# Kernel optimization log

Measured on AMD Instinct MI355X. Metric: run time of the kernel, lower is better.

## Reference

```python
import jax, jax.numpy as jnp
import numpy as np

N = 100000   # nodes
E = 1250000  # edges
G = 64       # graphs in batch
F_IN, H, NT, GT = 29, 64, 6, 4
L = 4        # num GCN layers


def setup_inputs() -> dict:
    key = jax.random.key(0)
    ks = jax.random.split(key, 14)
    s_in = 1.0 / np.sqrt(F_IN)
    s_h = 1.0 / np.sqrt(H)
    return {
        "x": jax.random.normal(ks[0], (N, F_IN), dtype=jnp.float32),
        "edge_index": jax.random.randint(ks[1], (2, E), 0, N, dtype=jnp.int64),
        "batch": jnp.sort(jax.random.randint(ks[2], (N,), 0, G, dtype=jnp.int64)),
        "encW": jax.random.uniform(ks[3], (F_IN, H), jnp.float32, -s_in, s_in),
        "encb": jax.random.uniform(ks[4], (H,), jnp.float32, -s_in, s_in),
        "convW": jax.random.uniform(ks[5], (L, H, H), jnp.float32, -s_h, s_h),
        "convb": jax.random.uniform(ks[6], (L, H), jnp.float32, -s_h, s_h),
        "nodeW": jax.random.uniform(ks[7], (H, NT), jnp.float32, -s_h, s_h),
        "nodeb": jax.random.uniform(ks[8], (NT,), jnp.float32, -s_h, s_h),
        "g1W": jax.random.uniform(ks[9], (H, H), jnp.float32, -s_h, s_h),
        "g1b": jax.random.uniform(ks[10], (H,), jnp.float32, -s_h, s_h),
        "g2W": jax.random.uniform(ks[11], (H, GT), jnp.float32, -s_h, s_h),
        "g2b": jax.random.uniform(ks[12], (GT,), jnp.float32, -s_h, s_h),
    }


def reference(x, edge_index, batch, encW, encb, convW, convb, nodeW, nodeb, g1W, g1b, g2W, g2b):
    # GCNConv with self-loops and symmetric normalization (PyG defaults)
    loop = jnp.arange(N, dtype=edge_index.dtype)
    row = jnp.concatenate([edge_index[0], loop])  # senders
    col = jnp.concatenate([edge_index[1], loop])  # receivers
    deg = jax.ops.segment_sum(jnp.ones_like(col, dtype=x.dtype), col, num_segments=N)
    dis = jnp.where(deg > 0, deg ** -0.5, 0.0)
    norm = (dis[row] * dis[col])[:, None]  # [E+N, 1]

    h = jax.nn.relu(x @ encW + encb)
    for i in range(L):
        hw = h @ convW[i]  # transform then propagate
        agg = jax.ops.segment_sum(hw[row] * norm, col, num_segments=N)
        h = jax.nn.relu(agg + convb[i])

    pred_node = h @ nodeW + nodeb

    counts = jax.ops.segment_sum(jnp.ones((N,), x.dtype), batch, num_segments=G)
    gemb = jax.ops.segment_sum(h, batch, num_segments=G) / jnp.maximum(counts, 1.0)[:, None]
    pred_global = jax.nn.relu(gemb @ g1W + g1b) @ g2W + g2b
    return (pred_node, pred_global)
```

## Files before the change

kernel.cpp:

```cpp
#include <hip/hip_runtime.h>
#include <hip/hip_fp16.h>

#define N_NODES 100000
#define N_EDGES 1250000
#define N_GRAPHS 64
#define F_INN 29
#define HD 64
#define NT 6
#define GT 4
#define NLAYERS 4
#define RECS_CAP 3000000
#define NBLK 1563
#define NBUK 782
#define HGRID 256
#define GB_BLOCKS 391
#define ENC_BLOCKS 6250
#define NH_BLOCKS 3125

typedef __attribute__((ext_vector_type(8))) _Float16 f16x8;
typedef __attribute__((ext_vector_type(4))) float f32x4;

__global__ void hist1_misc(const int* __restrict__ col, int* __restrict__ ghistT, int E,
                           const float* __restrict__ convW, uint4* __restrict__ wfrag,
                           __half* __restrict__ ht1, __half* __restrict__ ht2,
                           const int* __restrict__ batch, int* __restrict__ start) {
    __shared__ int lh[NBUK];
    int tid = threadIdx.x, b = blockIdx.x;
    if (b < HGRID) {
        for (int i = tid; i < NBUK; i += 256) lh[i] = 0;
        __syncthreads();
        for (int e = b * 256 + tid; e < E; e += HGRID * 256) atomicAdd(&lh[col[e] >> 7], 1);
        __syncthreads();
        for (int i = tid; i < NBUK; i += 256) ghistT[i * 256 + b] = lh[i];
    } else if (b < HGRID + 4) {
        int layer = b - HGRID;
        const float* W = convW + (size_t)layer * HD * HD;
        uint4* out = wfrag + (size_t)layer * 512;
        for (int s = tid; s < 512; s += 256) {
            int jt = s >> 7, ks = (s >> 6) & 1, l = s & 63;
            int j = jt * 16 + (l & 15);
            int k0 = ks * 32 + (l >> 4) * 8;
            __align__(16) __half hh[8];
            #pragma unroll
            for (int i = 0; i < 8; ++i) hh[i] = __float2half_rn(W[(size_t)(k0 + i) * HD + j]);
            out[s] = *reinterpret_cast<const uint4*>(hh);
        }
    } else if (b == HGRID + 4) {
        if (tid < HD) ht1[(size_t)N_NODES * HD + tid] = __float2half_rn(0.f);
        else if (tid < 2 * HD) ht2[(size_t)N_NODES * HD + (tid - HD)] = __float2half_rn(0.f);
    } else {
        int i = (b - HGRID - 5) * 256 + tid;
        if (i < N_NODES) {
            int bb = batch[i];
            if (i == 0) {
                for (int g = 0; g <= bb; ++g) start[g] = 0;
            } else {
                int pb = batch[i - 1];
                if (pb != bb) for (int g = pb + 1; g <= bb; ++g) start[g] = i;
            }
            if (i == N_NODES - 1) {
                for (int g = bb + 1; g <= N_GRAPHS; ++g) start[g] = N_NODES;
            }
        }
    }
}

__global__ void hist_colscan(int* __restrict__ ghistT, int* __restrict__ tot) {
    __shared__ int wsum[4];
    int k = blockIdx.x, tid = threadIdx.x;
    int v = ghistT[k * 256 + tid];
    int incl = v;
    int lane = tid & 63;
    #pragma unroll
    for (int off = 1; off < 64; off <<= 1) {
        int t = __shfl_up(incl, (unsigned)off, 64);
        if (lane >= off) incl += t;
    }
    if (lane == 63) wsum[tid >> 6] = incl;
    __syncthreads();
    int woff = 0;
    for (int w = 0; w < (tid >> 6); ++w) woff += wsum[w];
    ghistT[k * 256 + tid] = woff + incl - v;
    if (tid == 255) tot[k] = woff + incl;
}

__global__ void scan1(const int* __restrict__ in, int* __restrict__ out,
                      int* __restrict__ bsums, int n) {
    __shared__ int wsum[4];
    int tid = threadIdx.x;
    int base = blockIdx.x * 1024 + tid * 4;
    int v0 = (base + 0 < n) ? in[base + 0] : 0;
    int v1 = (base + 1 < n) ? in[base + 1] : 0;
    int v2 = (base + 2 < n) ? in[base + 2] : 0;
    int v3 = (base + 3 < n) ? in[base + 3] : 0;
    int tsum = v0 + v1 + v2 + v3;
    int incl = tsum;
    int lane = tid & 63;
    #pragma unroll
    for (int off = 1; off < 64; off <<= 1) {
        int t = __shfl_up(incl, (unsigned)off, 64);
        if (lane >= off) incl += t;
    }
    if (lane == 63) wsum[tid >> 6] = incl;
    __syncthreads();
    int woff = 0;
    for (int w = 0; w < (tid >> 6); ++w) woff += wsum[w];
    int run = woff + incl - tsum;
    if (base + 0 < n) out[base + 0] = run; run += v0;
    if (base + 1 < n) out[base + 1] = run; run += v1;
    if (base + 2 < n) out[base + 2] = run; run += v2;
    if (base + 3 < n) out[base + 3] = run;
    if (tid == 255) bsums[blockIdx.x] = woff + incl;
}

__global__ void scatter_buckets(const int* __restrict__ row, const int* __restrict__ col,
                                const int* __restrict__ ghistT, const int* __restrict__ boff,
                                unsigned* __restrict__ bke, int E) {
    __shared__ int cur[NBUK];
    int tid = threadIdx.x, b = blockIdx.x;
    for (int i = tid; i < NBUK; i += 256) cur[i] = ghistT[i * 256 + b] + boff[i];
    __syncthreads();
    for (int e = b * 256 + tid; e < E; e += HGRID * 256) {
        int c = col[e];
        int pos = atomicAdd(&cur[c >> 7], 1);
        bke[pos] = (unsigned)row[e] | ((unsigned)(c & 127) << 25);
    }
}

__global__ void bucket_count(const unsigned* __restrict__ bke, const int* __restrict__ boff,
                             int* __restrict__ cnt16, float* __restrict__ dis,
                             int* __restrict__ btot, int E) {
    __shared__ int lc[128];
    __shared__ int red[2];
    int k = blockIdx.x, tid = threadIdx.x;
    if (tid < 128) lc[tid] = 0;
    __syncthreads();
    int s = boff[k];
    int t = (k == NBUK - 1) ? E : boff[k + 1];
    for (int i = s + tid; i < t; i += 256) atomicAdd(&lc[bke[i] >> 25], 1);
    __syncthreads();
    int c16 = 0;
    if (tid < 128) {
        int node = k * 128 + tid;
        if (node < N_NODES) {
            int c = lc[tid];
            c16 = (c + 15) & ~15;
            cnt16[node] = c16;
            dis[node] = rsqrtf((float)(c + 1));
        }
        int sum = c16;
        #pragma unroll
        for (int off = 1; off < 64; off <<= 1) sum += __shfl_xor(sum, off, 64);
        if ((tid & 63) == 0) red[tid >> 6] = sum;
    }
    __syncthreads();
    if (tid == 0) btot[k] = red[0] + red[1];
}

__global__ void fill_enc(const unsigned* __restrict__ bke, const int* __restrict__ boff,
                         const int* __restrict__ bbase, const int* __restrict__ cnt16,
                         int* __restrict__ offs, int* __restrict__ srcs, int E,
                         const float* __restrict__ x, const float* __restrict__ encW,
                         const float* __restrict__ encb, const float* __restrict__ dis,
                         __half* __restrict__ ht) {
    int tid = threadIdx.x;
    int b = blockIdx.x;
    if (b < NBUK) {
        __shared__ int offsL[128];
        __shared__ int cur[128];
        __shared__ int wtot[2];
        int k = b;
        int v = 0, incl = 0;
        if (tid < 128) {
            int node = k * 128 + tid;
            v = (node < N_NODES) ? cnt16[node] : 0;
            incl = v;
            int lane = tid & 63;
            #pragma unroll
            for (int off = 1; off < 64; off <<= 1) {
                int t = __shfl_up(incl, (unsigned)off, 64);
                if (lane >= off) incl += t;
            }
            if (lane == 63) wtot[tid >> 6] = incl;
        }
        __syncthreads();
        if (tid < 128) {
            int w0 = (tid >= 64) ? wtot[0] : 0;
            int node = k * 128 + tid;
            int o = bbase[k] + w0 + incl - v;
            offsL[tid] = o;
            cur[tid] = 0;
            if (node < N_NODES) offs[node] = o;
        }
        __syncthreads();
        int s = boff[k];
        int t = (k == NBUK - 1) ? E : boff[k + 1];
        for (int i = s + tid; i < t; i += 256) {
            unsigned u = bke[i];
            int l = u >> 25;
            int r = atomicAdd(&cur[l], 1);
            srcs[offsL[l] + r] = (int)(u & 0x01FFFFFFu);
        }
        __syncthreads();
        if (tid < 128) {
            int node = k * 128 + tid;
            if (node < N_NODES) {
                int c = cur[tid];
                int c16 = (c + 15) & ~15;
                int base = offsL[tid];
                for (int p = base + c; p < base + c16; ++p) srcs[p] = N_NODES;
            }
        }
    } else {
        __shared__ float Ws[F_INN * HD];
        __shared__ float bs[HD];
        __shared__ float xs[16 * F_INN];
        for (int i = tid; i < F_INN * HD; i += 256) Ws[i] = encW[i];
        if (tid < HD) bs[tid] = encb[tid];
        int n0 = (b - NBUK) * 16;
        for (int i = tid; i < 16 * F_INN; i += 256) {
            int nn = n0 + i / F_INN;
            xs[i] = (nn < N_NODES) ? x[(size_t)nn * F_INN + (i % F_INN)] : 0.f;
        }
        __syncthreads();
        #pragma unroll
        for (int it = 0; it < 4; ++it) {
            int l = it * 4 + (tid >> 6);
            int j = tid & 63;
            int nn = n0 + l;
            if (nn < N_NODES) {
                float a = bs[j];
                #pragma unroll
                for (int k = 0; k < F_INN; ++k) a = fmaf(xs[l * F_INN + k], Ws[k * HD + j], a);
                ht[(size_t)nn * HD + j] = __float2half_rn(dis[nn] * fmaxf(a, 0.f));
            }
        }
    }
}


__device__ __forceinline__ float4 cvtrow(uint2 u) {
    float2 a = __half22float2(*reinterpret_cast<const __half2*>(&u.x));
    float2 b = __half22float2(*reinterpret_cast<const __half2*>(&u.y));
    return make_float4(a.x, a.y, b.x, b.y);
}

#define ROW16(src) (*reinterpret_cast<const uint2*>(&ht[(size_t)(src) * HD + fh]))
#define H2(u) (*reinterpret_cast<const __half2*>(&(u)))
#define ACC4T(r0, r1, r2, r3) { \
    __half2 ax = __hadd2(__hadd2(H2(r0.x), H2(r1.x)), __hadd2(H2(r2.x), H2(r3.x))); \
    __half2 ay = __hadd2(__hadd2(H2(r0.y), H2(r1.y)), __hadd2(H2(r2.y), H2(r3.y))); \
    float2 fx = __half22float2(ax); \
    float2 fy = __half22float2(ay); \
    acc.x += fx.x; acc.y += fx.y; acc.z += fy.x; acc.w += fy.y; }

__global__ void layer_kernel(const __half* __restrict__ ht,
                             const int* __restrict__ offs, const int* __restrict__ cnt16,
                             const int4* __restrict__ srcs4,
                             const float* __restrict__ dis,
                             const uint4* __restrict__ wfragL, const float* __restrict__ bias,
                             __half* __restrict__ hout, int scaleOut) {
    __shared__ uint4 WfS[512];
    __shared__ __half aggS[64 * 72];
    __shared__ int offsS[64];
    __shared__ int cntS[64];
    __shared__ float disS[64];
    __shared__ float biasS[64];
    int tid = threadIdx.x;
    int b = blockIdx.x;
    WfS[tid] = wfragL[tid];
    WfS[tid + 256] = wfragL[tid + 256];
    if (tid < 64) {
        int d = b * 64 + tid;
        biasS[tid] = bias[tid];
        if (d < N_NODES) {
            offsS[tid] = offs[d];
            cntS[tid] = cnt16[d];
            disS[tid] = dis[d];
        } else {
            offsS[tid] = offs[N_NODES - 1] + cnt16[N_NODES - 1];
            cntS[tid] = 0;
            disS[tid] = 0.f;
        }
    }
    __syncthreads();

    int wave = tid >> 6;
    int lane = tid & 63;
    int q = lane >> 4;
    int fh = (lane & 15) * 4;

    int l0 = wave * 16 + q * 4;
    {
        int nbase = b * 64 + l0;
        *reinterpret_cast<uint2*>(&aggS[(l0 + 0) * 72 + fh]) = ROW16(min(nbase + 0, N_NODES));
        *reinterpret_cast<uint2*>(&aggS[(l0 + 1) * 72 + fh]) = ROW16(min(nbase + 1, N_NODES));
        *reinterpret_cast<uint2*>(&aggS[(l0 + 2) * 72 + fh]) = ROW16(min(nbase + 2, N_NODES));
        *reinterpret_cast<uint2*>(&aggS[(l0 + 3) * 72 + fh]) = ROW16(min(nbase + 3, N_NODES));
    }
    int s = offsS[l0];
    int e = offsS[l0 + 3] + cntS[l0 + 3];
    int dcur = l0;
    int nb = offsS[l0] + cntS[l0];
    float4 acc = {0.f, 0.f, 0.f, 0.f};

    auto flush = [&](int d) {
        uint2 sv = *reinterpret_cast<uint2*>(&aggS[d * 72 + fh]);
        float4 sf = cvtrow(sv);
        acc.x += sf.x; acc.y += sf.y; acc.z += sf.z; acc.w += sf.w;
        __half2 h0 = __floats2half2_rn(acc.x, acc.y);
        __half2 h1 = __floats2half2_rn(acc.z, acc.w);
        uint2 w;
        w.x = *(unsigned*)&h0;
        w.y = *(unsigned*)&h1;
        *reinterpret_cast<uint2*>(&aggS[d * 72 + fh]) = w;
        acc = make_float4(0.f, 0.f, 0.f, 0.f);
    };

    int4 i0, i1, i2, i3;
    if (s < e) {
        int base = s >> 2;
        i0 = srcs4[base + 0];
        i1 = srcs4[base + 1];
        i2 = srcs4[base + 2];
        i3 = srcs4[base + 3];
    }
    for (int p = s; p < e; p += 16) {
        uint2 r0 = ROW16(i0.x), r1 = ROW16(i0.y), r2 = ROW16(i0.z), r3 = ROW16(i0.w);
        uint2 r4 = ROW16(i1.x), r5 = ROW16(i1.y), r6 = ROW16(i1.z), r7 = ROW16(i1.w);
        uint2 r8 = ROW16(i2.x), r9 = ROW16(i2.y), r10 = ROW16(i2.z), r11 = ROW16(i2.w);
        uint2 r12 = ROW16(i3.x), r13 = ROW16(i3.y), r14 = ROW16(i3.z), r15 = ROW16(i3.w);
        int pn = p + 16;
        if (pn < e) {
            int base = pn >> 2;
            i0 = srcs4[base + 0];
            i1 = srcs4[base + 1];
            i2 = srcs4[base + 2];
            i3 = srcs4[base + 3];
        }
        while (p >= nb) {
            flush(dcur);
            ++dcur;
            nb = offsS[dcur] + cntS[dcur];
        }
        ACC4T(r0, r1, r2, r3);
        ACC4T(r4, r5, r6, r7);
        ACC4T(r8, r9, r10, r11);
        ACC4T(r12, r13, r14, r15);
    }
    while (dcur <= l0 + 3) {
        flush(dcur);
        ++dcur;
    }

    f32x4 c0 = {0.f, 0.f, 0.f, 0.f}, c1 = c0, c2 = c0, c3 = c0;
    #pragma unroll
    for (int ks = 0; ks < 2; ++ks) {
        f16x8 a = *reinterpret_cast<const f16x8*>(
            &aggS[(wave * 16 + (lane & 15)) * 72 + ks * 32 + (lane >> 4) * 8]);
        f16x8 b0 = *reinterpret_cast<const f16x8*>(&WfS[(0 * 2 + ks) * 64 + lane]);
        c0 = __builtin_amdgcn_mfma_f32_16x16x32_f16(a, b0, c0, 0, 0, 0);
        f16x8 b1 = *reinterpret_cast<const f16x8*>(&WfS[(1 * 2 + ks) * 64 + lane]);
        c1 = __builtin_amdgcn_mfma_f32_16x16x32_f16(a, b1, c1, 0, 0, 0);
        f16x8 b2 = *reinterpret_cast<const f16x8*>(&WfS[(2 * 2 + ks) * 64 + lane]);
        c2 = __builtin_amdgcn_mfma_f32_16x16x32_f16(a, b2, c2, 0, 0, 0);
        f16x8 b3 = *reinterpret_cast<const f16x8*>(&WfS[(3 * 2 + ks) * 64 + lane]);
        c3 = __builtin_amdgcn_mfma_f32_16x16x32_f16(a, b3, c3, 0, 0, 0);
    }
    #pragma unroll
    for (int jt = 0; jt < 4; ++jt) {
        f32x4 c = (jt == 0) ? c0 : (jt == 1) ? c1 : (jt == 2) ? c2 : c3;
        int j = jt * 16 + (lane & 15);
        float bj = biasS[j];
        #pragma unroll
        for (int i = 0; i < 4; ++i) {
            int rl = wave * 16 + (lane >> 4) * 4 + i;
            int node = b * 64 + rl;
            if (node < N_NODES) {
                float dn = disS[rl];
                float o = fmaxf(fmaf(dn, c[i], bj), 0.f);
                if (scaleOut) o *= dn;
                hout[(size_t)node * HD + j] = __float2half_rn(o);
            }
        }
    }
}

__global__ void heads_kernel(const __half* __restrict__ h, const float* __restrict__ W,
                             const float* __restrict__ bb, float* __restrict__ out,
                             const int* __restrict__ start, float* __restrict__ gpart) {
    int tid = threadIdx.x;
    int b = blockIdx.x;
    if (b < NH_BLOCKS) {
        __shared__ float Ws[HD * NT];
        __shared__ float bs[NT];
        __shared__ float hs[32 * 65];
        for (int i = tid; i < HD * NT; i += 256) Ws[i] = W[i];
        if (tid < NT) bs[tid] = bb[tid];
        int n0 = b * 32;
        const unsigned* hrow = reinterpret_cast<const unsigned*>(&h[(size_t)n0 * HD]);
        for (int i = tid; i < 32 * HD / 2; i += 256) {
            unsigned u = hrow[i];
            float2 f = __half22float2(*reinterpret_cast<const __half2*>(&u));
            int el = i * 2;
            int row = el >> 6, colc = el & 63;
            hs[row * 65 + colc] = f.x;
            hs[row * 65 + colc + 1] = f.y;
        }
        __syncthreads();
        int l = tid >> 3, t = tid & 7;
        int nn = n0 + l;
        if (nn < N_NODES && t < NT) {
            float a = bs[t];
            #pragma unroll
            for (int k = 0; k < HD; ++k) a = fmaf(hs[l * 65 + k], Ws[k * NT + t], a);
            out[(size_t)nn * NT + t] = a;
        }
    } else {
        __shared__ float red[4][HD];
        int pb = b - NH_BLOCKS;
        int g = pb >> 2, q = pb & 3;
        int s0 = start[g], e0 = start[g + 1];
        int len = e0 - s0;
        int qs = s0 + (len * q) / 4;
        int qe = s0 + (len * (q + 1)) / 4;
        int wave = tid >> 6, lane = tid & 63;
        float acc = 0.f;
        for (int r = qs + wave; r < qe; r += 4) acc += __half2float(h[(size_t)r * HD + lane]);
        red[wave][lane] = acc;
        __syncthreads();
        if (wave == 0)
            gpart[(size_t)pb * HD + lane] =
                red[0][lane] + red[1][lane] + red[2][lane] + red[3][lane];
    }
}

__global__ void global_head(const float* __restrict__ gpart, const int* __restrict__ start,
                            const float* __restrict__ g1W, const float* __restrict__ g1b,
                            const float* __restrict__ g2W, const float* __restrict__ g2b,
                            float* __restrict__ out) {
    __shared__ float rS[HD];
    int g = blockIdx.x;
    int j = threadIdx.x;
    int cnt = start[g + 1] - start[g];
    float inv = 1.f / fmaxf((float)cnt, 1.f);
    rS[j] = (gpart[(size_t)(4 * g + 0) * HD + j] + gpart[(size_t)(4 * g + 1) * HD + j] +
             gpart[(size_t)(4 * g + 2) * HD + j] + gpart[(size_t)(4 * g + 3) * HD + j]) * inv;
    __syncthreads();
    float a = g1b[j];
    #pragma unroll
    for (int k = 0; k < HD; ++k) a = fmaf(rS[k], g1W[k * HD + j], a);
    a = fmaxf(a, 0.f);
    float o0 = a * g2W[j * GT + 0];
    float o1 = a * g2W[j * GT + 1];
    float o2 = a * g2W[j * GT + 2];
    float o3 = a * g2W[j * GT + 3];
    #pragma unroll
    for (int off = 1; off < 64; off <<= 1) {
        o0 += __shfl_xor(o0, off, 64);
        o1 += __shfl_xor(o1, off, 64);
        o2 += __shfl_xor(o2, off, 64);
        o3 += __shfl_xor(o3, off, 64);
    }
    if (j == 0) {
        out[g * GT + 0] = o0 + g2b[0];
        out[g * GT + 1] = o1 + g2b[1];
        out[g * GT + 2] = o2 + g2b[2];
        out[g * GT + 3] = o3 + g2b[3];
    }
}


extern "C" void kernel_launch(void* const* d_in, const int* in_sizes, int n_in,
                              void* d_out, int out_size, void* d_ws, size_t ws_size,
                              hipStream_t stream) {
    const float* x    = (const float*)d_in[0];
    const int*   ei   = (const int*)d_in[1];
    const int*   batch= (const int*)d_in[2];
    const float* encW = (const float*)d_in[3];
    const float* encb = (const float*)d_in[4];
    const float* convW= (const float*)d_in[5];
    const float* convb= (const float*)d_in[6];
    const float* nodeW= (const float*)d_in[7];
    const float* nodeb= (const float*)d_in[8];
    const float* g1W  = (const float*)d_in[9];
    const float* g1b  = (const float*)d_in[10];
    const float* g2W  = (const float*)d_in[11];
    const float* g2b  = (const float*)d_in[12];
    float* out = (float*)d_out;

    const int N = N_NODES, E = N_EDGES;

    char* ws = (char*)d_ws;
    size_t off = 0;
    auto alloc = [&](size_t bytes) -> void* {
        void* p = ws + off;
        off += (bytes + 255) & ~(size_t)255;
        return p;
    };
    int*    ghistT = (int*)alloc((size_t)NBUK * 256 * 4);
    int*    tot    = (int*)alloc((size_t)NBUK * 4);
    int*    boff   = (int*)alloc((size_t)NBUK * 4);
    int*    btot   = (int*)alloc((size_t)NBUK * 4);
    int*    bbase  = (int*)alloc((size_t)NBUK * 4);
    unsigned* bke  = (unsigned*)alloc((size_t)E * 4);
    int*    offs   = (int*)alloc((size_t)N * 4);
    int*    cnt16  = (int*)alloc((size_t)N * 4);
    float*  dis    = (float*)alloc((size_t)N * 4);
    int*    bsums  = (int*)alloc(256 * 4);
    int*    start  = (int*)alloc((size_t)(N_GRAPHS + 1) * 4);
    float*  gpart  = (float*)alloc((size_t)N_GRAPHS * 4 * HD * 4);
    uint4*  wfrag  = (uint4*)alloc((size_t)NLAYERS * 512 * 16);
    int*    srcs   = (int*)alloc((size_t)RECS_CAP * 4);
    __half* ht1    = (__half*)alloc((size_t)(N + 1) * HD * 2);
    __half* ht2    = (__half*)alloc((size_t)(N + 1) * HD * 2);

    hist1_misc<<<HGRID + 5 + GB_BLOCKS, 256, 0, stream>>>(ei + E, ghistT, E, convW, wfrag,
                                                          ht1, ht2, batch, start);
    hist_colscan<<<NBUK, 256, 0, stream>>>(ghistT, tot);
    scan1<<<1, 256, 0, stream>>>(tot, boff, bsums, NBUK);
    scatter_buckets<<<HGRID, 256, 0, stream>>>(ei, ei + E, ghistT, boff, bke, E);
    bucket_count<<<NBUK, 256, 0, stream>>>(bke, boff, cnt16, dis, btot, E);
    scan1<<<1, 256, 0, stream>>>(btot, bbase, bsums, NBUK);
    fill_enc<<<NBUK + ENC_BLOCKS, 256, 0, stream>>>(bke, boff, bbase, cnt16, offs, srcs, E,
                                                    x, encW, encb, dis, ht1);

    __half* hin = ht1;
    __half* hot = ht2;
    for (int i = 0; i < NLAYERS; ++i) {
        layer_kernel<<<NBLK, 256, 0, stream>>>(hin, offs, cnt16, (const int4*)srcs, dis,
                                               wfrag + (size_t)i * 512,
                                               convb + (size_t)i * HD,
                                               hot, (i < NLAYERS - 1) ? 1 : 0);
        __half* t = hin; hin = hot; hot = t;
    }

    heads_kernel<<<NH_BLOCKS + N_GRAPHS * 4, 256, 0, stream>>>(hin, nodeW, nodeb, out,
                                                               start, gpart);
    global_head<<<N_GRAPHS, 64, 0, stream>>>(gpart, start, g1W, g1b, g2W, g2b, out + (size_t)N * NT);
}
```

Before: 225.7 us.

## Fold bucket scans into consumer kernels and widen layer gathers to 16-byte rows

Removes the two single-block scan1 launches. Every scatter_buckets block now recomputes the bucket-offset prefix scan redundantly, and every fill_enc bucket block reduces btot up to its own index to find its base. Separately, the layer kernel's neighbour gather now loads 8 halves (16 bytes) per lane instead of 4. Two half-lane groups split the 16 edges and are combined with a shuffle at flush time. This trades launch overhead and serial tiny kernels for redundant scan work (fill_enc blocks read up to 782 values each) and extra shuffles, and it aims for fewer, wider memory transactions in the gather.

```diff
diff --git a/kernel.cpp b/kernel.cpp
--- a/kernel.cpp
+++ b/kernel.cpp
@@ -84,41 +84,43 @@
     if (tid == 255) tot[k] = woff + incl;
 }
 
-__global__ void scan1(const int* __restrict__ in, int* __restrict__ out,
-                      int* __restrict__ bsums, int n) {
+__global__ void scatter_buckets(const int* __restrict__ row, const int* __restrict__ col,
+                                const int* __restrict__ ghistT, const int* __restrict__ tot,
+                                int* __restrict__ boff,
+                                unsigned* __restrict__ bke, int E) {
+    __shared__ int boffL[NBUK];
+    __shared__ int cur[NBUK];
     __shared__ int wsum[4];
-    int tid = threadIdx.x;
-    int base = blockIdx.x * 1024 + tid * 4;
-    int v0 = (base + 0 < n) ? in[base + 0] : 0;
-    int v1 = (base + 1 < n) ? in[base + 1] : 0;
-    int v2 = (base + 2 < n) ? in[base + 2] : 0;
-    int v3 = (base + 3 < n) ? in[base + 3] : 0;
-    int tsum = v0 + v1 + v2 + v3;
-    int incl = tsum;
-    int lane = tid & 63;
-    #pragma unroll
-    for (int off = 1; off < 64; off <<= 1) {
-        int t = __shfl_up(incl, (unsigned)off, 64);
-        if (lane >= off) incl += t;
-    }
-    if (lane == 63) wsum[tid >> 6] = incl;
-    __syncthreads();
-    int woff = 0;
-    for (int w = 0; w < (tid >> 6); ++w) woff += wsum[w];
-    int run = woff + incl - tsum;
-    if (base + 0 < n) out[base + 0] = run; run += v0;
-    if (base + 1 < n) out[base + 1] = run; run += v1;
-    if (base + 2 < n) out[base + 2] = run; run += v2;
-    if (base + 3 < n) out[base + 3] = run;
-    if (tid == 255) bsums[blockIdx.x] = woff + incl;
-}
-
-__global__ void scatter_buckets(const int* __restrict__ row, const int* __restrict__ col,
-                                const int* __restrict__ ghistT, const int* __restrict__ boff,
-                                unsigned* __restrict__ bke, int E) {
-    __shared__ int cur[NBUK];
     int tid = threadIdx.x, b = blockIdx.x;
-    for (int i = tid; i < NBUK; i += 256) cur[i] = ghistT[i * 256 + b] + boff[i];
+    {
+        int base = tid * 4;
+        int v0 = (base + 0 < NBUK) ? tot[base + 0] : 0;
+        int v1 = (base + 1 < NBUK) ? tot[base + 1] : 0;
+        int v2 = (base + 2 < NBUK) ? tot[base + 2] : 0;
+        int v3 = (base + 3 < NBUK) ? tot[base + 3] : 0;
+        int tsum = v0 + v1 + v2 + v3;
+        int incl = tsum;
+        int lane = tid & 63;
+        #pragma unroll
+        for (int off = 1; off < 64; off <<= 1) {
+            int t = __shfl_up(incl, (unsigned)off, 64);
+            if (lane >= off) incl += t;
+        }
+        if (lane == 63) wsum[tid >> 6] = incl;
+        __syncthreads();
+        int woff = 0;
+        for (int w = 0; w < (tid >> 6); ++w) woff += wsum[w];
+        int run = woff + incl - tsum;
+        if (base + 0 < NBUK) boffL[base + 0] = run; run += v0;
+        if (base + 1 < NBUK) boffL[base + 1] = run; run += v1;
+        if (base + 2 < NBUK) boffL[base + 2] = run; run += v2;
+        if (base + 3 < NBUK) boffL[base + 3] = run;
+    }
+    __syncthreads();
+    for (int i = tid; i < NBUK; i += 256) {
+        cur[i] = ghistT[i * 256 + b] + boffL[i];
+        if (b == 0) boff[i] = boffL[i];
+    }
     __syncthreads();
     for (int e = b * 256 + tid; e < E; e += HGRID * 256) {
         int c = col[e];
@@ -158,7 +160,7 @@
 }
 
 __global__ void fill_enc(const unsigned* __restrict__ bke, const int* __restrict__ boff,
-                         const int* __restrict__ bbase, const int* __restrict__ cnt16,
+                         const int* __restrict__ btot, const int* __restrict__ cnt16,
                          int* __restrict__ offs, int* __restrict__ srcs, int E,
                          const float* __restrict__ x, const float* __restrict__ encW,
                          const float* __restrict__ encb, const float* __restrict__ dis,
@@ -169,7 +171,18 @@
         __shared__ int offsL[128];
         __shared__ int cur[128];
         __shared__ int wtot[2];
+        __shared__ int wred[4];
         int k = b;
+        int partial = 0;
+        for (int i = tid; i < k; i += 256) partial += btot[i];
+        {
+            int lane = tid & 63;
+            #pragma unroll
+            for (int off = 1; off < 64; off <<= 1) partial += __shfl_xor(partial, off, 64);
+            if (lane == 0) wred[tid >> 6] = partial;
+        }
+        __syncthreads();
+        int bbasek = wred[0] + wred[1] + wred[2] + wred[3];
         int v = 0, incl = 0;
         if (tid < 128) {
             int node = k * 128 + tid;
@@ -187,7 +200,7 @@
         if (tid < 128) {
             int w0 = (tid >= 64) ? wtot[0] : 0;
             int node = k * 128 + tid;
-            int o = bbase[k] + w0 + incl - v;
+            int o = bbasek + w0 + incl - v;
             offsL[tid] = o;
             cur[tid] = 0;
             if (node < N_NODES) offs[node] = o;
@@ -239,20 +252,14 @@
 }
 
 
-__device__ __forceinline__ float4 cvtrow(uint2 u) {
-    float2 a = __half22float2(*reinterpret_cast<const __half2*>(&u.x));
-    float2 b = __half22float2(*reinterpret_cast<const __half2*>(&u.y));
-    return make_float4(a.x, a.y, b.x, b.y);
-}
-
-#define ROW16(src) (*reinterpret_cast<const uint2*>(&ht[(size_t)(src) * HD + fh]))
 #define H2(u) (*reinterpret_cast<const __half2*>(&(u)))
-#define ACC4T(r0, r1, r2, r3) { \
-    __half2 ax = __hadd2(__hadd2(H2(r0.x), H2(r1.x)), __hadd2(H2(r2.x), H2(r3.x))); \
-    __half2 ay = __hadd2(__hadd2(H2(r0.y), H2(r1.y)), __hadd2(H2(r2.y), H2(r3.y))); \
-    float2 fx = __half22float2(ax); \
-    float2 fy = __half22float2(ay); \
-    acc.x += fx.x; acc.y += fx.y; acc.z += fy.x; acc.w += fy.y; }
+#define ROWQ(src) (*reinterpret_cast<const uint4*>(&ht[(size_t)(src) * HD + fh8]))
+#define ACCQ(c, idx0, idx1) { \
+    __half2 t0 = __hadd2(__hadd2(H2(r0.c), H2(r1.c)), __hadd2(H2(r2.c), H2(r3.c))); \
+    __half2 t1 = __hadd2(__hadd2(H2(r4.c), H2(r5.c)), __hadd2(H2(r6.c), H2(r7.c))); \
+    float2 f0 = __half22float2(t0); \
+    float2 f1 = __half22float2(t1); \
+    acc[idx0] += f0.x + f1.x; acc[idx1] += f0.y + f1.y; }
 
 __global__ void layer_kernel(const __half* __restrict__ ht,
                              const int* __restrict__ offs, const int* __restrict__ cnt16,
@@ -288,33 +295,53 @@
     int wave = tid >> 6;
     int lane = tid & 63;
     int q = lane >> 4;
-    int fh = (lane & 15) * 4;
+    int lane16 = lane & 15;
+    int sub = lane16 >> 3;
+    int fh8 = (lane16 & 7) * 8;
 
     int l0 = wave * 16 + q * 4;
     {
         int nbase = b * 64 + l0;
-        *reinterpret_cast<uint2*>(&aggS[(l0 + 0) * 72 + fh]) = ROW16(min(nbase + 0, N_NODES));
-        *reinterpret_cast<uint2*>(&aggS[(l0 + 1) * 72 + fh]) = ROW16(min(nbase + 1, N_NODES));
-        *reinterpret_cast<uint2*>(&aggS[(l0 + 2) * 72 + fh]) = ROW16(min(nbase + 2, N_NODES));
-        *reinterpret_cast<uint2*>(&aggS[(l0 + 3) * 72 + fh]) = ROW16(min(nbase + 3, N_NODES));
+        int d0 = sub * 2, d1 = sub * 2 + 1;
+        *reinterpret_cast<uint4*>(&aggS[(l0 + d0) * 72 + fh8]) =
+            *reinterpret_cast<const uint4*>(&ht[(size_t)min(nbase + d0, N_NODES) * HD + fh8]);
+        *reinterpret_cast<uint4*>(&aggS[(l0 + d1) * 72 + fh8]) =
+            *reinterpret_cast<const uint4*>(&ht[(size_t)min(nbase + d1, N_NODES) * HD + fh8]);
     }
     int s = offsS[l0];
     int e = offsS[l0 + 3] + cntS[l0 + 3];
     int dcur = l0;
     int nb = offsS[l0] + cntS[l0];
-    float4 acc = {0.f, 0.f, 0.f, 0.f};
+    float acc[8] = {0.f, 0.f, 0.f, 0.f, 0.f, 0.f, 0.f, 0.f};
 
     auto flush = [&](int d) {
-        uint2 sv = *reinterpret_cast<uint2*>(&aggS[d * 72 + fh]);
-        float4 sf = cvtrow(sv);
-        acc.x += sf.x; acc.y += sf.y; acc.z += sf.z; acc.w += sf.w;
-        __half2 h0 = __floats2half2_rn(acc.x, acc.y);
-        __half2 h1 = __floats2half2_rn(acc.z, acc.w);
-        uint2 w;
-        w.x = *(unsigned*)&h0;
-        w.y = *(unsigned*)&h1;
-        *reinterpret_cast<uint2*>(&aggS[d * 72 + fh]) = w;
-        acc = make_float4(0.f, 0.f, 0.f, 0.f);
+        float a0 = acc[0] + __shfl_xor(acc[0], 8, 64);
+        float a1 = acc[1] + __shfl_xor(acc[1], 8, 64);
+        float a2 = acc[2] + __shfl_xor(acc[2], 8, 64);
+        float a3 = acc[3] + __shfl_xor(acc[3], 8, 64);
+        float a4 = acc[4] + __shfl_xor(acc[4], 8, 64);
+        float a5 = acc[5] + __shfl_xor(acc[5], 8, 64);
+        float a6 = acc[6] + __shfl_xor(acc[6], 8, 64);
+        float a7 = acc[7] + __shfl_xor(acc[7], 8, 64);
+        if (sub == 0) {
+            uint4 sv = *reinterpret_cast<uint4*>(&aggS[d * 72 + fh8]);
+            float2 s0 = __half22float2(H2(sv.x));
+            float2 s1 = __half22float2(H2(sv.y));
+            float2 s2 = __half22float2(H2(sv.z));
+            float2 s3 = __half22float2(H2(sv.w));
+            __half2 h0 = __floats2half2_rn(a0 + s0.x, a1 + s0.y);
+            __half2 h1 = __floats2half2_rn(a2 + s1.x, a3 + s1.y);
+            __half2 h2 = __floats2half2_rn(a4 + s2.x, a5 + s2.y);
+            __half2 h3 = __floats2half2_rn(a6 + s3.x, a7 + s3.y);
+            uint4 w;
+            w.x = *(unsigned*)&h0;
+            w.y = *(unsigned*)&h1;
+            w.z = *(unsigned*)&h2;
+            w.w = *(unsigned*)&h3;
+            *reinterpret_cast<uint4*>(&aggS[d * 72 + fh8]) = w;
+        }
+        #pragma unroll
+        for (int i = 0; i < 8; ++i) acc[i] = 0.f;
     };
 
     int4 i0, i1, i2, i3;
@@ -326,10 +353,10 @@
         i3 = srcs4[base + 3];
     }
     for (int p = s; p < e; p += 16) {
-        uint2 r0 = ROW16(i0.x), r1 = ROW16(i0.y), r2 = ROW16(i0.z), r3 = ROW16(i0.w);
-        uint2 r4 = ROW16(i1.x), r5 = ROW16(i1.y), r6 = ROW16(i1.z), r7 = ROW16(i1.w);
-        uint2 r8 = ROW16(i2.x), r9 = ROW16(i2.y), r10 = ROW16(i2.z), r11 = ROW16(i2.w);
-        uint2 r12 = ROW16(i3.x), r13 = ROW16(i3.y), r14 = ROW16(i3.z), r15 = ROW16(i3.w);
+        int4 ia = sub ? i2 : i0;
+        int4 ib = sub ? i3 : i1;
+        uint4 r0 = ROWQ(ia.x), r1 = ROWQ(ia.y), r2 = ROWQ(ia.z), r3 = ROWQ(ia.w);
+        uint4 r4 = ROWQ(ib.x), r5 = ROWQ(ib.y), r6 = ROWQ(ib.z), r7 = ROWQ(ib.w);
         int pn = p + 16;
         if (pn < e) {
             int base = pn >> 2;
@@ -343,10 +370,10 @@
             ++dcur;
             nb = offsS[dcur] + cntS[dcur];
         }
-        ACC4T(r0, r1, r2, r3);
-        ACC4T(r4, r5, r6, r7);
-        ACC4T(r8, r9, r10, r11);
-        ACC4T(r12, r13, r14, r15);
+        ACCQ(x, 0, 1);
+        ACCQ(y, 2, 3);
+        ACCQ(z, 4, 5);
+        ACCQ(w, 6, 7);
     }
     while (dcur <= l0 + 3) {
         flush(dcur);
@@ -502,12 +529,10 @@
     int*    tot    = (int*)alloc((size_t)NBUK * 4);
     int*    boff   = (int*)alloc((size_t)NBUK * 4);
     int*    btot   = (int*)alloc((size_t)NBUK * 4);
-    int*    bbase  = (int*)alloc((size_t)NBUK * 4);
     unsigned* bke  = (unsigned*)alloc((size_t)E * 4);
     int*    offs   = (int*)alloc((size_t)N * 4);
     int*    cnt16  = (int*)alloc((size_t)N * 4);
     float*  dis    = (float*)alloc((size_t)N * 4);
-    int*    bsums  = (int*)alloc(256 * 4);
     int*    start  = (int*)alloc((size_t)(N_GRAPHS + 1) * 4);
     float*  gpart  = (float*)alloc((size_t)N_GRAPHS * 4 * HD * 4);
     uint4*  wfrag  = (uint4*)alloc((size_t)NLAYERS * 512 * 16);
@@ -518,11 +543,9 @@
     hist1_misc<<<HGRID + 5 + GB_BLOCKS, 256, 0, stream>>>(ei + E, ghistT, E, convW, wfrag,
                                                           ht1, ht2, batch, start);
     hist_colscan<<<NBUK, 256, 0, stream>>>(ghistT, tot);
-    scan1<<<1, 256, 0, stream>>>(tot, boff, bsums, NBUK);
-    scatter_buckets<<<HGRID, 256, 0, stream>>>(ei, ei + E, ghistT, boff, bke, E);
+    scatter_buckets<<<HGRID, 256, 0, stream>>>(ei, ei + E, ghistT, tot, boff, bke, E);
     bucket_count<<<NBUK, 256, 0, stream>>>(bke, boff, cnt16, dis, btot, E);
-    scan1<<<1, 256, 0, stream>>>(btot, bbase, bsums, NBUK);
-    fill_enc<<<NBUK + ENC_BLOCKS, 256, 0, stream>>>(bke, boff, bbase, cnt16, offs, srcs, E,
+    fill_enc<<<NBUK + ENC_BLOCKS, 256, 0, stream>>>(bke, boff, btot, cnt16, offs, srcs, E,
                                                     x, encW, encb, dis, ht1);
 
     __half* hin = ht1;
```

Result: faster. 207.5 us (median of 2 runs) (-8.1%).
